# Optimization experiments

Hardware: AMD Instinct MI355X
Metric: run time of the kernel (lower is better)

## Reference

```python
import jax, jax.numpy as jnp
import numpy as np

B, S, H, E = 8, 4096, 1024, 8
TEMPERATURE = 1.0


def setup_inputs() -> dict:
    key = jax.random.key(0)
    ks = jax.random.split(key, 7)
    s_h = 1.0 / np.sqrt(H).astype(np.float32)
    s_h2 = 1.0 / np.sqrt(H // 2).astype(np.float32)
    return {
        "hidden_states": jax.random.normal(ks[0], (B, S, H), jnp.float32),
        # routing_network: Linear(H, H//2) -> ReLU -> Linear(H//2, E)
        "W1": jax.random.normal(ks[1], (H, H // 2), jnp.float32) * s_h,
        "b1": jnp.zeros((H // 2,), jnp.float32),
        "W2": jax.random.normal(ks[2], (H // 2, E), jnp.float32) * s_h2,
        "b2": jnp.zeros((E,), jnp.float32),
        # per-expert dense transform (fixed stand-in for torch.randn-per-call)
        "expert_W": jax.random.normal(ks[3], (E, H, H), jnp.float32) * s_h,
        "expert_b": jax.random.normal(ks[4], (E, H), jnp.float32),
    }


def reference(hidden_states, W1, b1, W2, b2, expert_W, expert_b):
    # Routing network -> logits [B, S, E]
    h = jax.nn.relu(jnp.einsum("bsh,hf->bsf", hidden_states, W1) + b1)
    logits = jnp.einsum("bsf,fe->bse", h, W2) + b2
    probs = jax.nn.softmax(logits / TEMPERATURE, axis=-1)
    # top-1 expert per token (scores are NOT applied to output in the original)
    sel = jnp.argmax(probs, axis=-1)  # [B, S] int
    out = jnp.zeros_like(hidden_states)
    for e in range(E):  # small fixed loop over experts
        mask = (sel == e)[..., None].astype(hidden_states.dtype)  # [B, S, 1]
        xe = hidden_states * mask
        ye = jnp.einsum("bsh,hd->bsd", xe, expert_W[e]) + expert_b[e]
        out = out + ye * mask
    return out
```

## Files before the change

### kernel.cpp

```cpp
#include <hip/hip_runtime.h>
#include <hip/hip_bf16.h>
#include <stdint.h>

#define NTOK 32768
#define HD 1024
#define FD 512
#define NEXP 8
#define TAU 0.05f
#define TAU2 4e-4f

typedef __attribute__((ext_vector_type(8))) short short8;
typedef __attribute__((ext_vector_type(4))) float f32x4;

__device__ __forceinline__ short f2bh(float f) {
  uint32_t u = __float_as_uint(f);
  return (short)((u + 0x7fffu + ((u >> 16) & 1u)) >> 16);
}
__device__ __forceinline__ float bh2f(short h) {
  return __uint_as_float(((uint32_t)(uint16_t)h) << 16);
}

__device__ __forceinline__ void gl16(void* lds, const void* g) {
  __builtin_amdgcn_global_load_lds(
      (const __attribute__((address_space(1))) void*)g,
      (__attribute__((address_space(3))) void*)lds, 16, 0, 0);
}

__global__ __launch_bounds__(256) void k_convert(const float* __restrict__ x,
                                                 short* __restrict__ xbf) {
  size_t i = ((size_t)blockIdx.x * 256 + threadIdx.x) * 8;
  f32x4 v0 = *(const f32x4*)(x + i);
  f32x4 v1 = *(const f32x4*)(x + i + 4);
  short8 o;
#pragma unroll
  for (int q = 0; q < 4; ++q) { o[q] = f2bh(v0[q]); o[4 + q] = f2bh(v1[q]); }
  *(short8*)(xbf + i) = o;
}

__global__ __launch_bounds__(256) void k_transpose(
    const float* __restrict__ src, short* __restrict__ dst, int rows, int cols) {
  __shared__ float tile[32][33];
  size_t msz = (size_t)rows * cols;
  src += (size_t)blockIdx.z * msz;
  dst += (size_t)blockIdx.z * msz;
  int c0 = blockIdx.x * 32, r0 = blockIdx.y * 32;
  int tx = threadIdx.x & 31, ty = threadIdx.x >> 5;
#pragma unroll
  for (int i = 0; i < 32; i += 8)
    tile[ty + i][tx] = src[(size_t)(r0 + ty + i) * cols + c0 + tx];
  __syncthreads();
#pragma unroll
  for (int i = 0; i < 32; i += 8)
    dst[(size_t)(c0 + ty + i) * rows + r0 + tx] = f2bh(tile[tx][ty + i]);
}

__global__ __launch_bounds__(256) void k_transpose_split(
    const float* __restrict__ src, short* __restrict__ dstH,
    short* __restrict__ dstL, int rows, int cols) {
  __shared__ float tile[32][33];
  int c0 = blockIdx.x * 32, r0 = blockIdx.y * 32;
  int tx = threadIdx.x & 31, ty = threadIdx.x >> 5;
#pragma unroll
  for (int i = 0; i < 32; i += 8)
    tile[ty + i][tx] = src[(size_t)(r0 + ty + i) * cols + c0 + tx];
  __syncthreads();
#pragma unroll
  for (int i = 0; i < 32; i += 8) {
    float v = tile[tx][ty + i];
    short h = f2bh(v);
    size_t di = (size_t)(c0 + ty + i) * rows + r0 + tx;
    dstH[di] = h;
    dstL[di] = f2bh(v - bh2f(h));
  }
}

template <bool ABF>
__global__ __launch_bounds__(256) void k_gemm1(
    const short* __restrict__ xbf, const float* __restrict__ xf,
    const short* __restrict__ W1T, const float* __restrict__ b1,
    const float* __restrict__ W2, float* __restrict__ part) {
  __shared__ __align__(16) char smem[37888];
  short* As = (short*)smem;
  short* Bs = (short*)(smem + 8192);

  const int tid = threadIdx.x;
  const int lane = tid & 63, wave = tid >> 6;
  const int wr = wave >> 1, wc = wave & 1;
  const int fr = lane & 15, fg = lane >> 4;
  const int bx = ((blockIdx.x & 7) << 5) | (blockIdx.x >> 3);
  const int m0 = bx * 128, n0 = blockIdx.y * 128;
  const int by = blockIdx.y;

  const int off0 = wave * 1024 + lane * 16;
  const int off1 = off0 + 4096;
  const int r0 = off0 >> 6, c0 = (off0 & 63) >> 1;
  const int r1 = off1 >> 6, c1 = (off1 & 63) >> 1;
  const short* b0p = W1T + (size_t)(n0 + r0) * HD + c0;
  const short* b1p = W1T + (size_t)(n0 + r1) * HD + c1;
  char* ldsB0 = smem + 8192 + wave * 1024;
  char* ldsB1 = smem + 8192 + wave * 1024 + 4096;

  const short* a0p = nullptr; const short* a1p = nullptr;
  char* ldsA0 = smem + wave * 1024;
  char* ldsA1 = smem + wave * 1024 + 4096;
  const float* aF = nullptr;
  int ar = 0, ah = 0;
  if constexpr (ABF) {
    a0p = xbf + (size_t)(m0 + r0) * HD + c0;
    a1p = xbf + (size_t)(m0 + r1) * HD + c1;
  } else {
    ar = tid >> 1; ah = tid & 1;
    aF = xf + (size_t)(m0 + ar) * HD + ah * 16;
  }

  f32x4 acc[4][4];
#pragma unroll
  for (int i = 0; i < 4; ++i)
#pragma unroll
    for (int j = 0; j < 4; ++j) acc[i][j] = (f32x4){0.f, 0.f, 0.f, 0.f};

  for (int k0 = 0; k0 < HD; k0 += 32) {
    gl16(ldsB0, b0p + k0);
    gl16(ldsB1, b1p + k0);
    if constexpr (ABF) {
      gl16(ldsA0, a0p + k0);
      gl16(ldsA1, a1p + k0);
    } else {
      f32x4 u0 = *(const f32x4*)(aF + k0);
      f32x4 u1 = *(const f32x4*)(aF + k0 + 4);
      f32x4 u2 = *(const f32x4*)(aF + k0 + 8);
      f32x4 u3 = *(const f32x4*)(aF + k0 + 12);
      short8 s0, s1;
#pragma unroll
      for (int q = 0; q < 4; ++q) {
        s0[q] = f2bh(u0[q]); s0[4 + q] = f2bh(u1[q]);
        s1[q] = f2bh(u2[q]); s1[4 + q] = f2bh(u3[q]);
      }
      *(short8*)(As + ar * 32 + ah * 16) = s0;
      *(short8*)(As + ar * 32 + ah * 16 + 8) = s1;
    }
    __syncthreads();
    short8 af[4], bf[4];
#pragma unroll
    for (int i = 0; i < 4; ++i) {
      af[i] = *(const short8*)(As + (wr * 64 + i * 16 + fr) * 32 + fg * 8);
      bf[i] = *(const short8*)(Bs + (wc * 64 + i * 16 + fr) * 32 + fg * 8);
    }
#pragma unroll
    for (int i = 0; i < 4; ++i)
#pragma unroll
      for (int j = 0; j < 4; ++j)
        acc[i][j] = __builtin_amdgcn_mfma_f32_16x16x32_bf16(af[i], bf[j], acc[i][j], 0, 0, 0);
    __syncthreads();
  }

  float* hl64 = (float*)smem;
  float* W2c  = (float*)(smem + 33024);
  *(f32x4*)(W2c + tid * 4) = *(const f32x4*)(W2 + (size_t)n0 * NEXP + tid * 4);
  float b1j[4];
#pragma unroll
  for (int j = 0; j < 4; ++j) b1j[j] = b1[n0 + wc * 64 + j * 16 + fr];

  for (int p = 0; p < 2; ++p) {
    if (wr == p) {
#pragma unroll
      for (int i = 0; i < 4; ++i)
#pragma unroll
        for (int j = 0; j < 4; ++j) {
          int col = wc * 64 + j * 16 + fr;
#pragma unroll
          for (int q = 0; q < 4; ++q)
            hl64[(i * 16 + fg * 4 + q) * 129 + col] = fmaxf(acc[i][j][q] + b1j[j], 0.f);
        }
    }
    __syncthreads();
    if (tid < 128) {
      int r2 = tid & 63, eh = tid >> 6;
      const float* hrow = hl64 + r2 * 129;
      const float* wcp = W2c + eh * 4;
      float s0 = 0.f, s1 = 0.f, s2 = 0.f, s3 = 0.f;
      for (int f = 0; f < 128; ++f) {
        float hv = hrow[f];
        s0 += hv * wcp[f * 8 + 0];
        s1 += hv * wcp[f * 8 + 1];
        s2 += hv * wcp[f * 8 + 2];
        s3 += hv * wcp[f * 8 + 3];
      }
      float* pp = part + (size_t)(m0 + p * 64 + r2) * 32 + by * 8 + eh * 4;
      pp[0] = s0; pp[1] = s1; pp[2] = s2; pp[3] = s3;
    }
    __syncthreads();
  }
}

__global__ __launch_bounds__(256) void k_combine(
    const float* __restrict__ part, const float* __restrict__ b2,
    int* __restrict__ sel, int* __restrict__ flagged, int* __restrict__ nflag) {
  int t = blockIdx.x * 256 + threadIdx.x;
  const float* p = part + (size_t)t * 32;
  float lg[8];
#pragma unroll
  for (int e = 0; e < 8; ++e) lg[e] = p[e] + p[8 + e] + p[16 + e] + p[24 + e] + b2[e];
  int be = 0; float best = lg[0];
#pragma unroll
  for (int e = 1; e < 8; ++e) if (lg[e] > best) { best = lg[e]; be = e; }
  float second = -3.4e38f;
#pragma unroll
  for (int e = 0; e < 8; ++e) if (e != be && lg[e] > second) second = lg[e];
  sel[t] = be;
  if (best - second < TAU) {
    int ix = atomicAdd(nflag, 1);
    if (ix < NTOK) flagged[ix] = t;
  }
}

__global__ __launch_bounds__(256) void k_gemmR(
    const float* __restrict__ x, const short* __restrict__ W1hT,
    const short* __restrict__ W1lT, const float* __restrict__ b1,
    const float* __restrict__ W2, const int* __restrict__ flagged,
    const int* __restrict__ nflag, float* __restrict__ partR) {
  __shared__ __align__(16) char smem[37888];
  __shared__ int toks[128];
  short* Ah = (short*)smem;
  short* Al = (short*)(smem + 8192);

  int nf = *nflag; if (nf > NTOK) nf = NTOK;
  const int m0 = blockIdx.x * 128;
  if (m0 >= nf) return;
  const int tid = threadIdx.x;
  if (tid < 128) {
    int s = m0 + tid;
    toks[tid] = flagged[s < nf ? s : nf - 1];
  }
  __syncthreads();

  const int lane = tid & 63, wave = tid >> 6;
  const int wr = wave >> 1, wc = wave & 1;
  const int fr = lane & 15, fg = lane >> 4;
  const int n0 = blockIdx.y * 128;
  const int by = blockIdx.y;

  const int off0 = wave * 1024 + lane * 16;
  const int off1 = off0 + 4096;
  const int r0 = off0 >> 6, c0 = (off0 & 63) >> 1;
  const int r1 = off1 >> 6, c1 = (off1 & 63) >> 1;
  const short* bh0p = W1hT + (size_t)(n0 + r0) * HD + c0;
  const short* bh1p = W1hT + (size_t)(n0 + r1) * HD + c1;
  const short* bl0p = W1lT + (size_t)(n0 + r0) * HD + c0;
  const short* bl1p = W1lT + (size_t)(n0 + r1) * HD + c1;
  char* ldsBh0 = smem + 16384 + wave * 1024;
  char* ldsBh1 = smem + 16384 + wave * 1024 + 4096;
  char* ldsBl0 = smem + 24576 + wave * 1024;
  char* ldsBl1 = smem + 24576 + wave * 1024 + 4096;
  const int ar = tid >> 1, ah2 = tid & 1;
  const float* aF = x + (size_t)toks[ar] * HD + ah2 * 16;

  f32x4 acc[4][4];
#pragma unroll
  for (int i = 0; i < 4; ++i)
#pragma unroll
    for (int j = 0; j < 4; ++j) acc[i][j] = (f32x4){0.f, 0.f, 0.f, 0.f};

  for (int k0 = 0; k0 < HD; k0 += 32) {
    gl16(ldsBh0, bh0p + k0);
    gl16(ldsBh1, bh1p + k0);
    gl16(ldsBl0, bl0p + k0);
    gl16(ldsBl1, bl1p + k0);
    f32x4 u0 = *(const f32x4*)(aF + k0);
    f32x4 u1 = *(const f32x4*)(aF + k0 + 4);
    f32x4 u2 = *(const f32x4*)(aF + k0 + 8);
    f32x4 u3 = *(const f32x4*)(aF + k0 + 12);
    short8 sh0, sh1, sl0, sl1;
#pragma unroll
    for (int q = 0; q < 4; ++q) {
      { float f = u0[q]; short h = f2bh(f); sh0[q]     = h; sl0[q]     = f2bh(f - bh2f(h)); }
      { float f = u1[q]; short h = f2bh(f); sh0[4 + q] = h; sl0[4 + q] = f2bh(f - bh2f(h)); }
      { float f = u2[q]; short h = f2bh(f); sh1[q]     = h; sl1[q]     = f2bh(f - bh2f(h)); }
      { float f = u3[q]; short h = f2bh(f); sh1[4 + q] = h; sl1[4 + q] = f2bh(f - bh2f(h)); }
    }
    *(short8*)(Ah + ar * 32 + ah2 * 16)     = sh0;
    *(short8*)(Ah + ar * 32 + ah2 * 16 + 8) = sh1;
    *(short8*)(Al + ar * 32 + ah2 * 16)     = sl0;
    *(short8*)(Al + ar * 32 + ah2 * 16 + 8) = sl1;
    __syncthreads();
    short8 af[4], alf[4], bf[4], blf[4];
#pragma unroll
    for (int i = 0; i < 4; ++i) {
      int row = (wr * 64 + i * 16 + fr) * 32 + fg * 8;
      af[i]  = *(const short8*)(Ah + row);
      alf[i] = *(const short8*)(Al + row);
      int rowb = (wc * 64 + i * 16 + fr) * 32 + fg * 8;
      bf[i]  = *(const short8*)((short*)(smem + 16384) + rowb);
      blf[i] = *(const short8*)((short*)(smem + 24576) + rowb);
    }
#pragma unroll
    for (int i = 0; i < 4; ++i)
#pragma unroll
      for (int j = 0; j < 4; ++j) {
        acc[i][j] = __builtin_amdgcn_mfma_f32_16x16x32_bf16(af[i],  bf[j],  acc[i][j], 0, 0, 0);
        acc[i][j] = __builtin_amdgcn_mfma_f32_16x16x32_bf16(af[i],  blf[j], acc[i][j], 0, 0, 0);
        acc[i][j] = __builtin_amdgcn_mfma_f32_16x16x32_bf16(alf[i], bf[j],  acc[i][j], 0, 0, 0);
      }
    __syncthreads();
  }

  float* hl64 = (float*)smem;
  float* W2c  = (float*)(smem + 33024);
  *(f32x4*)(W2c + tid * 4) = *(const f32x4*)(W2 + (size_t)n0 * NEXP + tid * 4);
  float b1j[4];
#pragma unroll
  for (int j = 0; j < 4; ++j) b1j[j] = b1[n0 + wc * 64 + j * 16 + fr];

  for (int p = 0; p < 2; ++p) {
    if (wr == p) {
#pragma unroll
      for (int i = 0; i < 4; ++i)
#pragma unroll
        for (int j = 0; j < 4; ++j) {
          int col = wc * 64 + j * 16 + fr;
#pragma unroll
          for (int q = 0; q < 4; ++q)
            hl64[(i * 16 + fg * 4 + q) * 129 + col] = fmaxf(acc[i][j][q] + b1j[j], 0.f);
        }
    }
    __syncthreads();
    if (tid < 128) {
      int r2 = tid & 63, eh = tid >> 6;
      const float* hrow = hl64 + r2 * 129;
      const float* wcp = W2c + eh * 4;
      float s0 = 0.f, s1 = 0.f, s2 = 0.f, s3 = 0.f;
      for (int f = 0; f < 128; ++f) {
        float hv = hrow[f];
        s0 += hv * wcp[f * 8 + 0];
        s1 += hv * wcp[f * 8 + 1];
        s2 += hv * wcp[f * 8 + 2];
        s3 += hv * wcp[f * 8 + 3];
      }
      float* pp = partR + (size_t)(m0 + p * 64 + r2) * 32 + by * 8 + eh * 4;
      pp[0] = s0; pp[1] = s1; pp[2] = s2; pp[3] = s3;
    }
    __syncthreads();
  }
}

__global__ __launch_bounds__(256) void k_combineR(
    const float* __restrict__ partR, const float* __restrict__ b2,
    const int* __restrict__ flagged, const int* __restrict__ nflag,
    int* __restrict__ sel, int* __restrict__ flagged2, int* __restrict__ nflag2) {
  int nf = *nflag; if (nf > NTOK) nf = NTOK;
  int s = blockIdx.x * 256 + threadIdx.x;
  if (s >= nf) return;
  int t = flagged[s];
  const float* p = partR + (size_t)s * 32;
  float lg[8];
#pragma unroll
  for (int e = 0; e < 8; ++e) lg[e] = p[e] + p[8 + e] + p[16 + e] + p[24 + e] + b2[e];
  int be = 0; float best = lg[0];
#pragma unroll
  for (int e = 1; e < 8; ++e) if (lg[e] > best) { best = lg[e]; be = e; }
  float second = -3.4e38f;
#pragma unroll
  for (int e = 0; e < 8; ++e) if (e != be && lg[e] > second) second = lg[e];
  sel[t] = be;
  if (best - second < TAU2) {
    int ix = atomicAdd(nflag2, 1);
    if (ix < NTOK) flagged2[ix] = t;
  }
}

__global__ __launch_bounds__(256) void k_recomputeB(
    const float* __restrict__ x, const float* __restrict__ W1,
    const float* __restrict__ b1, const float* __restrict__ W2,
    const float* __restrict__ b2, const int* __restrict__ flagged2,
    const int* __restrict__ nflag2, int* __restrict__ sel) {
  __shared__ float xs[1024];
  __shared__ double hs[512];
  __shared__ double red[8][32];
  __shared__ double lgd[8];
  int nf = *nflag2; if (nf > NTOK) nf = NTOK;
  const int tid = threadIdx.x;
  for (int ti = blockIdx.x; ti < nf; ti += gridDim.x) {
    int t = flagged2[ti];
    __syncthreads();
    for (int q = tid; q < 1024; q += 256) xs[q] = x[(size_t)t * HD + q];
    __syncthreads();
    int f0 = tid * 2;
    double a0 = 0.0, a1 = 0.0;
    for (int h = 0; h < 1024; h += 4) {
      float2 w0 = *(const float2*)(W1 + (size_t)(h + 0) * FD + f0);
      float2 w1 = *(const float2*)(W1 + (size_t)(h + 1) * FD + f0);
      float2 w2 = *(const float2*)(W1 + (size_t)(h + 2) * FD + f0);
      float2 w3 = *(const float2*)(W1 + (size_t)(h + 3) * FD + f0);
      double x0 = (double)xs[h], x1 = (double)xs[h + 1];
      double x2 = (double)xs[h + 2], x3 = (double)xs[h + 3];
      a0 += x0 * (double)w0.x; a1 += x0 * (double)w0.y;
      a0 += x1 * (double)w1.x; a1 += x1 * (double)w1.y;
      a0 += x2 * (double)w2.x; a1 += x2 * (double)w2.y;
      a0 += x3 * (double)w3.x; a1 += x3 * (double)w3.y;
    }
    a0 += (double)b1[f0]; a1 += (double)b1[f0 + 1];
    hs[f0]     = a0 > 0.0 ? a0 : 0.0;
    hs[f0 + 1] = a1 > 0.0 ? a1 : 0.0;
    __syncthreads();
    {
      int e = tid >> 5, c = tid & 31;
      int fb = c * 16;
      double s = 0.0;
#pragma unroll
      for (int ff = 0; ff < 16; ++ff)
        s += hs[fb + ff] * (double)W2[(size_t)(fb + ff) * 8 + e];
      red[e][c] = s;
    }
    __syncthreads();
    if (tid < 8) {
      double s = 0.0;
#pragma unroll
      for (int c = 0; c < 32; ++c) s += red[tid][c];
      lgd[tid] = s + (double)b2[tid];
    }
    __syncthreads();
    if (tid == 0) {
      int be = 0; double best = lgd[0];
#pragma unroll
      for (int e = 1; e < 8; ++e) if (lgd[e] > best) { best = lgd[e]; be = e; }
      sel[t] = be;
    }
    __syncthreads();
  }
}

__global__ __launch_bounds__(256) void k_compact(
    const int* __restrict__ sel, int* __restrict__ cnt, int* __restrict__ list) {
  __shared__ int wcnt[4][8];
  __shared__ int woff[4][8];
  __shared__ int bbase[8];
  const int tid = threadIdx.x, lane = tid & 63, wave = tid >> 6;
  const int t = blockIdx.x * 256 + tid;
  const int e = sel[t];
  const unsigned long long ltmask = (1ull << lane) - 1ull;
  int rank = 0;
#pragma unroll
  for (int e2 = 0; e2 < 8; ++e2) {
    unsigned long long m = __ballot(e == e2);
    if (e2 == e) rank = __popcll(m & ltmask);
    if (lane == 0) wcnt[wave][e2] = __popcll(m);
  }
  __syncthreads();
  if (tid < 8) {
    int s0 = wcnt[0][tid], s1 = wcnt[1][tid], s2 = wcnt[2][tid], s3 = wcnt[3][tid];
    woff[0][tid] = 0; woff[1][tid] = s0; woff[2][tid] = s0 + s1; woff[3][tid] = s0 + s1 + s2;
    bbase[tid] = atomicAdd(&cnt[tid], s0 + s1 + s2 + s3);
  }
  __syncthreads();
  list[(size_t)e * NTOK + bbase[e] + woff[wave][e] + rank] = t;
}

__global__ void k_build_desc(const int* __restrict__ cnt, int* __restrict__ desc,
                             int* __restrict__ ntl) {
  if (threadIdx.x == 0 && blockIdx.x == 0) {
    int n = 0;
    for (int e = 0; e < 8; ++e) {
      int m = (cnt[e] + 127) >> 7;
      for (int i = 0; i < m; ++i) desc[n++] = (e << 16) | i;
    }
    *ntl = n;
  }
}

template <bool ABF>
__global__ __launch_bounds__(256) void k_gemm2(
    const short* __restrict__ xbf, const float* __restrict__ xf,
    const short* __restrict__ WexpT, const float* __restrict__ expert_b,
    const int* __restrict__ cnt, const int* __restrict__ list,
    const int* __restrict__ desc, const int* __restrict__ ntl,
    float* __restrict__ out) {
  __shared__ __align__(16) short As[128 * 32];
  __shared__ __align__(16) short Bs[128 * 32];
  __shared__ int toks[128];
  const int bx = (blockIdx.x % 8) * 33 + blockIdx.x / 8;
  if (bx >= *ntl) return;
  int dsc = desc[bx];
  int e = dsc >> 16, mt = dsc & 0xffff;
  int ce = cnt[e];
  int mb = mt * 128;
  int rows = ce - mb; if (rows > 128) rows = 128;

  const int tid = threadIdx.x;
  if (tid < 128) {
    int idx = mb + tid;
    toks[tid] = list[(size_t)e * NTOK + (idx < ce ? idx : ce - 1)];
  }
  __syncthreads();

  const int lane = tid & 63, wave = tid >> 6;
  const int wr = wave >> 1, wc = wave & 1;
  const int fr = lane & 15, fg = lane >> 4;
  const int n0 = blockIdx.y * 128;

  const int off0 = wave * 1024 + lane * 16;
  const int off1 = off0 + 4096;
  const int r0 = off0 >> 6, c0 = (off0 & 63) >> 1;
  const int r1 = off1 >> 6, c1 = (off1 & 63) >> 1;
  const size_t ebase = (size_t)e << 20;
  const short* b0p = WexpT + ebase + (size_t)(n0 + r0) * HD + c0;
  const short* b1p = WexpT + ebase + (size_t)(n0 + r1) * HD + c1;
  char* ldsA0 = (char*)As + wave * 1024;
  char* ldsA1 = (char*)As + wave * 1024 + 4096;
  char* ldsB0 = (char*)Bs + wave * 1024;
  char* ldsB1 = (char*)Bs + wave * 1024 + 4096;

  const short* a0p = nullptr; const short* a1p = nullptr;
  const float* aF = nullptr;
  int ar = 0, ah = 0;
  if constexpr (ABF) {
    a0p = xbf + (size_t)toks[r0] * HD + c0;
    a1p = xbf + (size_t)toks[r1] * HD + c1;
  } else {
    ar = tid >> 1; ah = tid & 1;
    aF = xf + (size_t)toks[ar] * HD + ah * 16;
  }

  f32x4 acc[4][4];
#pragma unroll
  for (int i = 0; i < 4; ++i)
#pragma unroll
    for (int j = 0; j < 4; ++j) acc[i][j] = (f32x4){0.f, 0.f, 0.f, 0.f};

  for (int k0 = 0; k0 < HD; k0 += 32) {
    gl16(ldsB0, b0p + k0);
    gl16(ldsB1, b1p + k0);
    if constexpr (ABF) {
      gl16(ldsA0, a0p + k0);
      gl16(ldsA1, a1p + k0);
    } else {
      f32x4 u0 = *(const f32x4*)(aF + k0);
      f32x4 u1 = *(const f32x4*)(aF + k0 + 4);
      f32x4 u2 = *(const f32x4*)(aF + k0 + 8);
      f32x4 u3 = *(const f32x4*)(aF + k0 + 12);
      short8 s0, s1;
#pragma unroll
      for (int q = 0; q < 4; ++q) {
        s0[q] = f2bh(u0[q]); s0[4 + q] = f2bh(u1[q]);
        s1[q] = f2bh(u2[q]); s1[4 + q] = f2bh(u3[q]);
      }
      *(short8*)(As + ar * 32 + ah * 16) = s0;
      *(short8*)(As + ar * 32 + ah * 16 + 8) = s1;
    }
    __syncthreads();
    short8 af[4], bf[4];
#pragma unroll
    for (int i = 0; i < 4; ++i) {
      af[i] = *(const short8*)(As + (wr * 64 + i * 16 + fr) * 32 + fg * 8);
      bf[i] = *(const short8*)(Bs + (wc * 64 + i * 16 + fr) * 32 + fg * 8);
    }
#pragma unroll
    for (int i = 0; i < 4; ++i)
#pragma unroll
      for (int j = 0; j < 4; ++j)
        acc[i][j] = __builtin_amdgcn_mfma_f32_16x16x32_bf16(af[i], bf[j], acc[i][j], 0, 0, 0);
    __syncthreads();
  }

  float ebv[4];
#pragma unroll
  for (int j = 0; j < 4; ++j) ebv[j] = expert_b[e * HD + n0 + wc * 64 + j * 16 + fr];
#pragma unroll
  for (int i = 0; i < 4; ++i)
#pragma unroll
    for (int j = 0; j < 4; ++j) {
      int col = n0 + wc * 64 + j * 16 + fr;
#pragma unroll
      for (int q = 0; q < 4; ++q) {
        int rr = wr * 64 + i * 16 + fg * 4 + q;
        if (rr < rows) out[(size_t)toks[rr] * HD + col] = acc[i][j][q] + ebv[j];
      }
    }
}

extern "C" void kernel_launch(void* const* d_in, const int* in_sizes, int n_in,
                              void* d_out, int out_size, void* d_ws, size_t ws_size,
                              hipStream_t stream) {
  const float* x  = (const float*)d_in[0];
  const float* W1 = (const float*)d_in[1];
  const float* b1 = (const float*)d_in[2];
  const float* W2 = (const float*)d_in[3];
  const float* b2 = (const float*)d_in[4];
  const float* eW = (const float*)d_in[5];
  const float* eb = (const float*)d_in[6];
  float* out = (float*)d_out;
  char* ws = (char*)d_ws;

  const size_t XBF_BYTES = (size_t)NTOK * HD * 2;
  size_t need_rest = 16777216ull + 1048576 + 4194304 + 131072 * 3 + 1048576 + 4096;
  bool big = ws_size >= XBF_BYTES + need_rest;

  size_t off = 0;
  short* xbf = nullptr;
  if (big) { xbf = (short*)ws; off += XBF_BYTES; }
  short* WexpT  = (short*)(ws + off); off += 16777216;
  short* W1T    = (short*)(ws + off); off += 1048576;
  float* part   = (float*)(ws + off); off += 4194304;
  int* sel      = (int*)(ws + off); off += 131072;
  int* flagged  = (int*)(ws + off); off += 131072;
  int* flagged2 = (int*)(ws + off); off += 131072;
  int* list     = (int*)(ws + off); off += 1048576;
  int* cnt      = (int*)(ws + off); off += 32;
  int* nflag    = (int*)(ws + off); off += 4;
  int* ntl      = (int*)(ws + off); off += 4;
  int* nflag2   = (int*)(ws + off); off += 24;
  int* desc     = (int*)(ws + off); off += 1088;
  if (ws_size < off) return;

  short* W1lT = (short*)list;

  hipMemsetAsync(cnt, 0, 44, stream);

  dim3 b256(256);
  if (big) k_convert<<<dim3(16384), b256, 0, stream>>>(x, xbf);
  k_transpose_split<<<dim3(16, 32), b256, 0, stream>>>(W1, W1T, W1lT, 1024, 512);
  k_transpose<<<dim3(32, 32, 8), b256, 0, stream>>>(eW, WexpT, 1024, 1024);
  if (big)
    k_gemm1<true><<<dim3(256, 4), b256, 0, stream>>>(xbf, nullptr, W1T, b1, W2, part);
  else
    k_gemm1<false><<<dim3(256, 4), b256, 0, stream>>>(nullptr, x, W1T, b1, W2, part);
  k_combine<<<dim3(128), b256, 0, stream>>>(part, b2, sel, flagged, nflag);
  k_gemmR<<<dim3(256, 4), b256, 0, stream>>>(x, W1T, W1lT, b1, W2, flagged, nflag, part);
  k_combineR<<<dim3(128), b256, 0, stream>>>(part, b2, flagged, nflag, sel, flagged2, nflag2);
  k_recomputeB<<<dim3(128), b256, 0, stream>>>(x, W1, b1, W2, b2, flagged2, nflag2, sel);
  k_compact<<<dim3(128), b256, 0, stream>>>(sel, cnt, list);
  k_build_desc<<<dim3(1), dim3(64), 0, stream>>>(cnt, desc, ntl);
  if (big)
    k_gemm2<true><<<dim3(264, 8), b256, 0, stream>>>(xbf, nullptr, WexpT, eb, cnt, list, desc, ntl, out);
  else
    k_gemm2<false><<<dim3(264, 8), b256, 0, stream>>>(nullptr, x, WexpT, eb, cnt, list, desc, ntl, out);
}
```

Measured before the change: 356.5 us.

## Double-buffer LDS staging in both GEMMs and use MFMA for the routing second layer

Both GEMM kernels now keep two LDS buffers and issue the global-to-LDS loads for the next K tile before running MFMAs on the current one. This gives one barrier per tile instead of two and overlaps memory latency with compute. The routing GEMM epilogue also stops using a scalar fp32 loop over 128 threads for the H/2→E projection. It instead writes ReLU outputs and W2 as bf16 into padded LDS and runs a 16x16x32 MFMA with zero-padded expert columns. This lowers precision of the routing logits, which could change argmax on near ties, and raises LDS use per block.

Result: no change. 362.5 us (+1.7%).

```diff
diff --git a/kernel.cpp b/kernel.cpp
--- a/kernel.cpp
+++ b/kernel.cpp
@@ -79,9 +79,7 @@
     const short* __restrict__ xbf, const float* __restrict__ xf,
     const short* __restrict__ W1T, const float* __restrict__ b1,
     const float* __restrict__ W2, float* __restrict__ part) {
-  __shared__ __align__(16) char smem[37888];
-  short* As = (short*)smem;
-  short* Bs = (short*)(smem + 8192);
+  __shared__ __align__(16) char smem[39168];
 
   const int tid = threadIdx.x;
   const int lane = tid & 63, wave = tid >> 6;
@@ -92,17 +90,12 @@
   const int by = blockIdx.y;
 
   const int off0 = wave * 1024 + lane * 16;
-  const int off1 = off0 + 4096;
   const int r0 = off0 >> 6, c0 = (off0 & 63) >> 1;
-  const int r1 = off1 >> 6, c1 = (off1 & 63) >> 1;
+  const int r1 = r0 + 64, c1 = c0;
   const short* b0p = W1T + (size_t)(n0 + r0) * HD + c0;
   const short* b1p = W1T + (size_t)(n0 + r1) * HD + c1;
-  char* ldsB0 = smem + 8192 + wave * 1024;
-  char* ldsB1 = smem + 8192 + wave * 1024 + 4096;
 
   const short* a0p = nullptr; const short* a1p = nullptr;
-  char* ldsA0 = smem + wave * 1024;
-  char* ldsA1 = smem + wave * 1024 + 4096;
   const float* aF = nullptr;
   int ar = 0, ah = 0;
   if constexpr (ABF) {
@@ -119,12 +112,13 @@
 #pragma unroll
     for (int j = 0; j < 4; ++j) acc[i][j] = (f32x4){0.f, 0.f, 0.f, 0.f};
 
-  for (int k0 = 0; k0 < HD; k0 += 32) {
-    gl16(ldsB0, b0p + k0);
-    gl16(ldsB1, b1p + k0);
+  auto STAGE = [&](int kt, int b) {
+    int k0 = kt * 32;
+    gl16(smem + 16384 + b * 8192 + wave * 1024, b0p + k0);
+    gl16(smem + 16384 + b * 8192 + 4096 + wave * 1024, b1p + k0);
     if constexpr (ABF) {
-      gl16(ldsA0, a0p + k0);
-      gl16(ldsA1, a1p + k0);
+      gl16(smem + b * 8192 + wave * 1024, a0p + k0);
+      gl16(smem + b * 8192 + 4096 + wave * 1024, a1p + k0);
     } else {
       f32x4 u0 = *(const f32x4*)(aF + k0);
       f32x4 u1 = *(const f32x4*)(aF + k0 + 4);
@@ -136,10 +130,14 @@
         s0[q] = f2bh(u0[q]); s0[4 + q] = f2bh(u1[q]);
         s1[q] = f2bh(u2[q]); s1[4 + q] = f2bh(u3[q]);
       }
+      short* As = (short*)(smem + b * 8192);
       *(short8*)(As + ar * 32 + ah * 16) = s0;
       *(short8*)(As + ar * 32 + ah * 16 + 8) = s1;
     }
-    __syncthreads();
+  };
+  auto COMPUTE = [&](int b) {
+    const short* As = (const short*)(smem + b * 8192);
+    const short* Bs = (const short*)(smem + 16384 + b * 8192);
     short8 af[4], bf[4];
 #pragma unroll
     for (int i = 0; i < 4; ++i) {
@@ -151,45 +149,55 @@
 #pragma unroll
       for (int j = 0; j < 4; ++j)
         acc[i][j] = __builtin_amdgcn_mfma_f32_16x16x32_bf16(af[i], bf[j], acc[i][j], 0, 0, 0);
-    __syncthreads();
-  }
-
-  float* hl64 = (float*)smem;
-  float* W2c  = (float*)(smem + 33024);
-  *(f32x4*)(W2c + tid * 4) = *(const f32x4*)(W2 + (size_t)n0 * NEXP + tid * 4);
+  };
+
+  STAGE(0, 0);
+  __syncthreads();
+#pragma unroll 1
+  for (int kt = 0; kt < 32; kt += 2) {
+    if (kt + 1 < 32) STAGE(kt + 1, 1);
+    COMPUTE(0);
+    __syncthreads();
+    if (kt + 2 < 32) STAGE(kt + 2, 0);
+    COMPUTE(1);
+    __syncthreads();
+  }
+
+  short* hbf = (short*)smem;
+  short* W2b = (short*)(smem + 34816);
   float b1j[4];
 #pragma unroll
   for (int j = 0; j < 4; ++j) b1j[j] = b1[n0 + wc * 64 + j * 16 + fr];
-
-  for (int p = 0; p < 2; ++p) {
-    if (wr == p) {
-#pragma unroll
-      for (int i = 0; i < 4; ++i)
-#pragma unroll
-        for (int j = 0; j < 4; ++j) {
-          int col = wc * 64 + j * 16 + fr;
-#pragma unroll
-          for (int q = 0; q < 4; ++q)
-            hl64[(i * 16 + fg * 4 + q) * 129 + col] = fmaxf(acc[i][j][q] + b1j[j], 0.f);
-        }
-    }
-    __syncthreads();
-    if (tid < 128) {
-      int r2 = tid & 63, eh = tid >> 6;
-      const float* hrow = hl64 + r2 * 129;
-      const float* wcp = W2c + eh * 4;
-      float s0 = 0.f, s1 = 0.f, s2 = 0.f, s3 = 0.f;
-      for (int f = 0; f < 128; ++f) {
-        float hv = hrow[f];
-        s0 += hv * wcp[f * 8 + 0];
-        s1 += hv * wcp[f * 8 + 1];
-        s2 += hv * wcp[f * 8 + 2];
-        s3 += hv * wcp[f * 8 + 3];
-      }
-      float* pp = part + (size_t)(m0 + p * 64 + r2) * 32 + by * 8 + eh * 4;
-      pp[0] = s0; pp[1] = s1; pp[2] = s2; pp[3] = s3;
-    }
-    __syncthreads();
+  for (int q = tid; q < 2048; q += 256) {
+    int col = q >> 7, k = q & 127;
+    W2b[col * 136 + k] = (col < 8) ? f2bh(W2[(size_t)(n0 + k) * 8 + col]) : (short)0;
+  }
+#pragma unroll
+  for (int i = 0; i < 4; ++i)
+#pragma unroll
+    for (int j = 0; j < 4; ++j) {
+      int col = wc * 64 + j * 16 + fr;
+#pragma unroll
+      for (int q = 0; q < 4; ++q)
+        hbf[(wr * 64 + i * 16 + fg * 4 + q) * 136 + col] =
+            f2bh(fmaxf(acc[i][j][q] + b1j[j], 0.f));
+    }
+  __syncthreads();
+#pragma unroll
+  for (int rg = 0; rg < 2; ++rg) {
+    int row16 = wave * 32 + rg * 16;
+    f32x4 accl = (f32x4){0.f, 0.f, 0.f, 0.f};
+#pragma unroll
+    for (int kk = 0; kk < 4; ++kk) {
+      short8 a = *(const short8*)(hbf + (row16 + fr) * 136 + kk * 32 + fg * 8);
+      short8 b = *(const short8*)(W2b + fr * 136 + kk * 32 + fg * 8);
+      accl = __builtin_amdgcn_mfma_f32_16x16x32_bf16(a, b, accl, 0, 0, 0);
+    }
+    if (fr < 8) {
+      float* pp = part + (size_t)(m0 + row16 + fg * 4) * 32 + by * 8 + fr;
+#pragma unroll
+      for (int q = 0; q < 4; ++q) pp[(size_t)q * 32] = accl[q];
+    }
   }
 }
 
@@ -474,8 +482,7 @@
     const int* __restrict__ cnt, const int* __restrict__ list,
     const int* __restrict__ desc, const int* __restrict__ ntl,
     float* __restrict__ out) {
-  __shared__ __align__(16) short As[128 * 32];
-  __shared__ __align__(16) short Bs[128 * 32];
+  __shared__ __align__(16) char smem[32768];
   __shared__ int toks[128];
   const int bx = (blockIdx.x % 8) * 33 + blockIdx.x / 8;
   if (bx >= *ntl) return;
@@ -498,16 +505,11 @@
   const int n0 = blockIdx.y * 128;
 
   const int off0 = wave * 1024 + lane * 16;
-  const int off1 = off0 + 4096;
   const int r0 = off0 >> 6, c0 = (off0 & 63) >> 1;
-  const int r1 = off1 >> 6, c1 = (off1 & 63) >> 1;
+  const int r1 = r0 + 64, c1 = c0;
   const size_t ebase = (size_t)e << 20;
   const short* b0p = WexpT + ebase + (size_t)(n0 + r0) * HD + c0;
   const short* b1p = WexpT + ebase + (size_t)(n0 + r1) * HD + c1;
-  char* ldsA0 = (char*)As + wave * 1024;
-  char* ldsA1 = (char*)As + wave * 1024 + 4096;
-  char* ldsB0 = (char*)Bs + wave * 1024;
-  char* ldsB1 = (char*)Bs + wave * 1024 + 4096;
 
   const short* a0p = nullptr; const short* a1p = nullptr;
   const float* aF = nullptr;
@@ -526,12 +528,13 @@
 #pragma unroll
     for (int j = 0; j < 4; ++j) acc[i][j] = (f32x4){0.f, 0.f, 0.f, 0.f};
 
-  for (int k0 = 0; k0 < HD; k0 += 32) {
-    gl16(ldsB0, b0p + k0);
-    gl16(ldsB1, b1p + k0);
+  auto STAGE = [&](int kt, int b) {
+    int k0 = kt * 32;
+    gl16(smem + 16384 + b * 8192 + wave * 1024, b0p + k0);
+    gl16(smem + 16384 + b * 8192 + 4096 + wave * 1024, b1p + k0);
     if constexpr (ABF) {
-      gl16(ldsA0, a0p + k0);
-      gl16(ldsA1, a1p + k0);
+      gl16(smem + b * 8192 + wave * 1024, a0p + k0);
+      gl16(smem + b * 8192 + 4096 + wave * 1024, a1p + k0);
     } else {
       f32x4 u0 = *(const f32x4*)(aF + k0);
       f32x4 u1 = *(const f32x4*)(aF + k0 + 4);
@@ -543,10 +546,14 @@
         s0[q] = f2bh(u0[q]); s0[4 + q] = f2bh(u1[q]);
         s1[q] = f2bh(u2[q]); s1[4 + q] = f2bh(u3[q]);
       }
+      short* As = (short*)(smem + b * 8192);
       *(short8*)(As + ar * 32 + ah * 16) = s0;
       *(short8*)(As + ar * 32 + ah * 16 + 8) = s1;
     }
-    __syncthreads();
+  };
+  auto COMPUTE = [&](int b) {
+    const short* As = (const short*)(smem + b * 8192);
+    const short* Bs = (const short*)(smem + 16384 + b * 8192);
     short8 af[4], bf[4];
 #pragma unroll
     for (int i = 0; i < 4; ++i) {
@@ -558,6 +565,17 @@
 #pragma unroll
       for (int j = 0; j < 4; ++j)
         acc[i][j] = __builtin_amdgcn_mfma_f32_16x16x32_bf16(af[i], bf[j], acc[i][j], 0, 0, 0);
+  };
+
+  STAGE(0, 0);
+  __syncthreads();
+#pragma unroll 1
+  for (int kt = 0; kt < 32; kt += 2) {
+    if (kt + 1 < 32) STAGE(kt + 1, 1);
+    COMPUTE(0);
+    __syncthreads();
+    if (kt + 2 < 32) STAGE(kt + 2, 0);
+    COMPUTE(1);
     __syncthreads();
   }
 
```
